# Kernel optimization log

Hardware: AMD Instinct MI355X
Metric: run time of the kernel (lower is better)

The kernel has to match this reference:

```python
import jax, jax.numpy as jnp
import numpy as np

N_NODES = 50000
N_EDGES = 800000
NUM_IN, NUM_HID, NUM_OUT = 512, 256, 64
EPS = 1e-12


def agnn_conv(x, src, dst, beta, num_nodes):
    # PyG AGNNConv: score(j->i) = beta * cos(x_i, x_j); softmax over incoming
    # edges of each target node i; out_i = sum_j alpha_ij * x_j.
    norm = jnp.maximum(jnp.linalg.norm(x, axis=1, keepdims=True), EPS)
    xn = x / norm                                      # [N, H]
    scores = beta * jnp.sum(xn[dst] * xn[src], axis=1)  # [E]
    m = jax.ops.segment_max(scores, dst, num_segments=num_nodes)
    e = jnp.exp(scores - m[dst])
    s = jax.ops.segment_sum(e, dst, num_segments=num_nodes)
    alpha = e / s[dst]                                  # [E]
    return jax.ops.segment_sum(alpha[:, None] * x[src], dst, num_segments=num_nodes)


def setup_inputs() -> dict:
    key = jax.random.key(0)
    ks = jax.random.split(key, 7)
    x = jax.random.normal(ks[0], (N_NODES, NUM_IN), dtype=jnp.float32)
    edge_index = jax.random.randint(ks[1], (2, N_EDGES), 0, N_NODES, dtype=jnp.int64)
    w1 = jax.random.normal(ks[2], (NUM_HID, NUM_IN), dtype=jnp.float32) / np.sqrt(NUM_IN)
    b1 = jnp.zeros((NUM_HID,), dtype=jnp.float32)
    beta2 = jnp.ones((1,), dtype=jnp.float32)
    w2 = jax.random.normal(ks[3], (NUM_OUT, NUM_HID), dtype=jnp.float32) / np.sqrt(NUM_HID)
    b2 = jnp.zeros((NUM_OUT,), dtype=jnp.float32)
    return {"x": x, "edge_index": edge_index, "w1": w1, "b1": b1,
            "beta2": beta2, "w2": w2, "b2": b2}


def reference(x, edge_index, w1, b1, beta2, w2, b2):
    n = x.shape[0]
    # add self-loops (PyG AGNNConv default add_self_loops=True)
    loops = jnp.arange(n, dtype=edge_index.dtype)
    src = jnp.concatenate([edge_index[0], loops])
    dst = jnp.concatenate([edge_index[1], loops])

    h = jax.nn.relu(x @ w1.T + b1)                       # [N, H] (eval: dropout = id)
    h = agnn_conv(h, src, dst, jnp.float32(1.0), n)      # prop1, fixed beta=1
    z1 = h
    h = agnn_conv(h, src, dst, beta2[0], n)              # prop2, learnable beta
    z2 = h
    logits = h @ w2.T + b2                               # [N, C]
    return (z1, z2, jax.nn.log_softmax(logits, axis=1))
```

## Files before the change

### kernel.cpp

```cpp
#include <hip/hip_runtime.h>

#define N_NODES 50000
#define N_EDGES 800000
#define ETOT (N_EDGES + N_NODES)
#define DIN 512
#define HID 256
#define NOUT 64
#define SCAN_CHUNK 2048

typedef __attribute__((ext_vector_type(8))) short short8;
typedef __attribute__((ext_vector_type(4))) float f32x4;
typedef __attribute__((ext_vector_type(4))) unsigned short us4;
typedef __attribute__((ext_vector_type(4))) unsigned int u32x4;

__device__ __forceinline__ unsigned short f2bf(float f) {
  union { float f; unsigned u; } x; x.f = f;
  unsigned r = x.u + 0x7fff + ((x.u >> 16) & 1);
  return (unsigned short)(r >> 16);
}
__device__ __forceinline__ float bf2f(unsigned short b) {
  return __uint_as_float(((unsigned)b) << 16);
}
__device__ __forceinline__ unsigned cvtpk(float a, float b) {
  unsigned r;
  asm("v_cvt_pk_bf16_f32 %0, %1, %2" : "=v"(r) : "v"(a), "v"(b));
  return r;
}

#define AS1(p) ((const __attribute__((address_space(1))) unsigned int*)(p))
#define AS3(p) ((__attribute__((address_space(3))) unsigned int*)(p))

__device__ __forceinline__ int edge_at(const void* ei, long long idx, int is32) {
  if (is32) return ((const int*)ei)[idx];
  return (int)((const long long*)ei)[idx];
}

__global__ void initK(const void* ei, int* cursor, int* flag,
                      const float* __restrict__ w1, unsigned short* __restrict__ wb) {
  int i = blockIdx.x * blockDim.x + threadIdx.x;
  if (i < N_NODES) cursor[i] = 1;
  if (i < (HID * DIN) / 8) {
    const float* src = w1 + i * 8;
    float4 v0 = ((const float4*)src)[0];
    float4 v1 = ((const float4*)src)[1];
    short8 s;
    s[0] = f2bf(v0.x); s[1] = f2bf(v0.y); s[2] = f2bf(v0.z); s[3] = f2bf(v0.w);
    s[4] = f2bf(v1.x); s[5] = f2bf(v1.y); s[6] = f2bf(v1.z); s[7] = f2bf(v1.w);
    *(short8*)(wb + i * 8) = s;
  }
  if (blockIdx.x == 0 && threadIdx.x < 64) {
    int lane = threadIdx.x;
    bool bad = false;
#pragma unroll
    for (int j = 0; j < 32; ++j) {
      long long v = ((const long long*)ei)[lane * 32 + j];
      bad |= (v < 0 || v >= N_NODES);
    }
    bool anybad = __any(bad);
    if (lane == 0) *flag = anybad ? 1 : 0;
  }
}

__global__ void histK(const void* ei, const int* flag, int* cursor) {
  int e = blockIdx.x * blockDim.x + threadIdx.x;
  if (e >= N_EDGES) return;
  int f = *flag;
  int d = edge_at(ei, (long long)N_EDGES + e, f);
  atomicAdd(&cursor[d], 1);
}

__global__ void scan1K(const int* counts, int* excl, int* bsums) {
  __shared__ int sdata[256];
  int base = blockIdx.x * SCAN_CHUNK;
  int t = threadIdx.x;
  int local[8];
  int sum = 0;
#pragma unroll
  for (int j = 0; j < 8; ++j) {
    int idx = base + t * 8 + j;
    int v = (idx < N_NODES) ? counts[idx] : 0;
    local[j] = sum;
    sum += v;
  }
  sdata[t] = sum;
  __syncthreads();
  for (int off = 1; off < 256; off <<= 1) {
    int v = (t >= off) ? sdata[t - off] : 0;
    __syncthreads();
    sdata[t] += v;
    __syncthreads();
  }
  int texcl = (t == 0) ? 0 : sdata[t - 1];
#pragma unroll
  for (int j = 0; j < 8; ++j) {
    int idx = base + t * 8 + j;
    if (idx < N_NODES) excl[idx] = texcl + local[j];
  }
  if (t == 255) bsums[blockIdx.x] = sdata[255];
}

__global__ void scan2K(int* bsums, int nb) {
  if (threadIdx.x == 0 && blockIdx.x == 0) {
    int run = 0;
    for (int i = 0; i < nb; ++i) { int v = bsums[i]; bsums[i] = run; run += v; }
  }
}

__global__ void scan3K(int* row_ptr, const int* bsums, int* cursor) {
  int i = blockIdx.x * blockDim.x + threadIdx.x;
  if (i < N_NODES) {
    int v = row_ptr[i] + bsums[i >> 11];
    row_ptr[i] = v;
    cursor[i] = v;
    if (i == 0) row_ptr[N_NODES] = ETOT;
  }
}

__global__ void scatterK(const void* ei, const int* flag, int* cursor, int* col) {
  int e = blockIdx.x * blockDim.x + threadIdx.x;
  if (e < N_EDGES) {
    int f = *flag;
    int s = edge_at(ei, e, f);
    int d = edge_at(ei, (long long)N_EDGES + e, f);
    int pos = atomicAdd(&cursor[d], 1);
    col[pos] = s;
  } else if (e < N_EDGES + N_NODES) {
    int i = e - N_EDGES;
    int pos = atomicAdd(&cursor[i], 1);
    col[pos] = i;
  }
}

__global__ __launch_bounds__(256) void gemm1MF(const float* __restrict__ A,
                                               const unsigned short* __restrict__ Bb,
                                               const float* __restrict__ bias,
                                               unsigned short* __restrict__ C) {
  __shared__ float As[128 * 64];
  __shared__ short Bs[128 * 64];
  int t = threadIdx.x;
  int wv = t >> 6, ln = t & 63;
  int wr = wv >> 1, wc = wv & 1;
  int row0 = blockIdx.x * 128;
  int col0 = blockIdx.y * 128;

  const float* aptr[8];
#pragma unroll
  for (int i = 0; i < 8; ++i) {
    int chunk = i * 4 + wv;
    int r = chunk * 4 + (ln >> 4);
    int gr = row0 + r;
    if (gr >= N_NODES) gr = N_NODES - 1;
    aptr[i] = &A[(long long)gr * DIN + (((ln & 15) ^ (r & 7)) << 2)];
  }
  const unsigned short* bptr[4];
#pragma unroll
  for (int i = 0; i < 4; ++i) {
    int chunk = i * 4 + wv;
    int r = chunk * 8 + (ln >> 3);
    bptr[i] = &Bb[(long long)(col0 + r) * DIN + (((ln & 7) ^ (r & 7)) << 3)];
  }

  f32x4 acc[4][4];
#pragma unroll
  for (int mi = 0; mi < 4; ++mi)
#pragma unroll
    for (int ni = 0; ni < 4; ++ni) acc[mi][ni] = (f32x4){0.f, 0.f, 0.f, 0.f};

  int g = ln >> 4;
  int fr = ln & 15;

  for (int k0 = 0; k0 < DIN; k0 += 64) {
#pragma unroll
    for (int i = 0; i < 8; ++i)
      __builtin_amdgcn_global_load_lds(AS1(aptr[i] + k0),
                                       AS3(&As[(i * 4 + wv) * 256]), 16, 0, 0);
#pragma unroll
    for (int i = 0; i < 4; ++i)
      __builtin_amdgcn_global_load_lds(AS1(bptr[i] + k0),
                                       AS3(&Bs[(i * 4 + wv) * 512]), 16, 0, 0);
    __syncthreads();

#pragma unroll
    for (int kk = 0; kk < 2; ++kk) {
      short8 af[4], bfr[4];
#pragma unroll
      for (int mi = 0; mi < 4; ++mi) {
        int r = wr * 64 + mi * 16 + fr;
        int s0 = kk * 8 + ((2 * g) ^ (r & 7));
        int s1 = kk * 8 + ((2 * g + 1) ^ (r & 7));
        f32x4 a0 = *(const f32x4*)&As[r * 64 + s0 * 4];
        f32x4 a1 = *(const f32x4*)&As[r * 64 + s1 * 4];
        u32x4 pk;
        pk.x = cvtpk(a0[0], a0[1]);
        pk.y = cvtpk(a0[2], a0[3]);
        pk.z = cvtpk(a1[0], a1[1]);
        pk.w = cvtpk(a1[2], a1[3]);
        af[mi] = __builtin_bit_cast(short8, pk);
      }
#pragma unroll
      for (int ni = 0; ni < 4; ++ni) {
        int c = wc * 64 + ni * 16 + fr;
        int slot = (kk * 4 + g) ^ (c & 7);
        bfr[ni] = *(const short8*)&Bs[c * 64 + slot * 8];
      }
#pragma unroll
      for (int mi = 0; mi < 4; ++mi)
#pragma unroll
        for (int ni = 0; ni < 4; ++ni)
          acc[mi][ni] = __builtin_amdgcn_mfma_f32_16x16x32_bf16(af[mi], bfr[ni], acc[mi][ni], 0, 0, 0);
    }
    __syncthreads();
  }

  int fq = ln >> 4;
#pragma unroll
  for (int ni = 0; ni < 4; ++ni) {
    int colv = col0 + wc * 64 + ni * 16 + fr;
    float bv = bias[colv];
#pragma unroll
    for (int mi = 0; mi < 4; ++mi) {
#pragma unroll
      for (int j = 0; j < 4; ++j) {
        int row = row0 + wr * 64 + mi * 16 + fq * 4 + j;
        if (row < N_NODES)
          C[(long long)row * HID + colv] = f2bf(fmaxf(acc[mi][ni][j] + bv, 0.f));
      }
    }
  }
}

__global__ __launch_bounds__(256) void normBF(const unsigned short* __restrict__ hb,
                                              float* __restrict__ invn) {
  int w = (blockIdx.x * 256 + threadIdx.x) >> 6;
  int lane = threadIdx.x & 63;
  if (w >= N_NODES) return;
  us4 v = *(const us4*)&hb[(long long)w * HID + lane * 4];
  float x = bf2f(v.x), y = bf2f(v.y), z = bf2f(v.z), ww = bf2f(v.w);
  float s = x * x + y * y + z * z + ww * ww;
#pragma unroll
  for (int off = 32; off >= 1; off >>= 1) s += __shfl_xor(s, off);
  if (lane == 0) invn[w] = 1.0f / fmaxf(sqrtf(s), 1e-12f);
}

__global__ __launch_bounds__(256) void convK(const unsigned short* __restrict__ hb,
                                             const float* __restrict__ invn,
                                             const int* __restrict__ row_ptr,
                                             const int* __restrict__ col,
                                             const float* __restrict__ beta_ptr,
                                             float* __restrict__ hout,
                                             unsigned short* __restrict__ hout_bf) {
  int w = (blockIdx.x * 256 + threadIdx.x) >> 6;
  int lane = threadIdx.x & 63;
  if (w >= N_NODES) return;
  int g = lane >> 4;
  int sub = lane & 15;
  float beta = beta_ptr ? beta_ptr[0] : 1.0f;
  float babs = fabsf(beta);

  const unsigned short* hrow = &hb[(long long)w * HID + sub * 16];
  short8 hia = *(const short8*)hrow;
  short8 hib = *(const short8*)(hrow + 8);
  float hi[16];
#pragma unroll
  for (int q = 0; q < 8; ++q) {
    hi[q] = bf2f((unsigned short)hia[q]);
    hi[8 + q] = bf2f((unsigned short)hib[q]);
  }
  float scale_i = invn[w] * beta;

  int e0 = row_ptr[w], e1 = row_ptr[w + 1];
  int nit = (e1 - e0 + 3) >> 2;
  float Z = 0.f;
  float acc[16];
#pragma unroll
  for (int q = 0; q < 16; ++q) acc[q] = 0.f;

  for (int it = 0; it < nit; ++it) {
    int ee = e0 + it * 4 + g;
    bool valid = ee < e1;
    int s = col[valid ? ee : (e1 - 1)];
    float is = invn[s];
    const unsigned short* hj = &hb[(long long)s * HID + sub * 16];
    short8 ja = *(const short8*)hj;
    short8 jb = *(const short8*)(hj + 8);
    float hjf[16];
#pragma unroll
    for (int q = 0; q < 8; ++q) {
      hjf[q] = bf2f((unsigned short)ja[q]);
      hjf[8 + q] = bf2f((unsigned short)jb[q]);
    }
    float p = 0.f;
#pragma unroll
    for (int q = 0; q < 16; ++q) p += hi[q] * hjf[q];
    p += __shfl_xor(p, 1);
    p += __shfl_xor(p, 2);
    p += __shfl_xor(p, 4);
    p += __shfl_xor(p, 8);
    float sc = p * scale_i * is;
    float wt = valid ? __expf(sc - babs) : 0.f;
    Z += wt;
#pragma unroll
    for (int q = 0; q < 16; ++q) acc[q] += wt * hjf[q];
  }

#pragma unroll
  for (int q = 0; q < 16; ++q) {
    acc[q] += __shfl_xor(acc[q], 16);
    acc[q] += __shfl_xor(acc[q], 32);
  }
  Z += __shfl_xor(Z, 16);
  Z += __shfl_xor(Z, 32);
  float r = 1.0f / Z;

  if (g == 0) {
    float* po = &hout[(long long)w * HID + sub * 16];
#pragma unroll
    for (int q4 = 0; q4 < 4; ++q4) {
      float4 o;
      o.x = acc[q4 * 4 + 0] * r;
      o.y = acc[q4 * 4 + 1] * r;
      o.z = acc[q4 * 4 + 2] * r;
      o.w = acc[q4 * 4 + 3] * r;
      *(float4*)&po[q4 * 4] = o;
    }
  } else if (g == 1 && hout_bf) {
    unsigned short* pb = &hout_bf[(long long)w * HID + sub * 16];
#pragma unroll
    for (int q4 = 0; q4 < 4; ++q4) {
      us4 ob;
      ob.x = f2bf(acc[q4 * 4 + 0] * r);
      ob.y = f2bf(acc[q4 * 4 + 1] * r);
      ob.z = f2bf(acc[q4 * 4 + 2] * r);
      ob.w = f2bf(acc[q4 * 4 + 3] * r);
      *(us4*)&pb[q4 * 4] = ob;
    }
  }
}

__global__ __launch_bounds__(256) void headK2(const float* __restrict__ Z,
                                              const float* __restrict__ W,
                                              const float* __restrict__ bias,
                                              float* __restrict__ out) {
  __shared__ float smem[2 * 32 * 68];
  float* As = smem;
  float* Bs = smem + 32 * 68;
  int t = threadIdx.x;
  int tx = t & 15, ty = t >> 4;
  int row0 = blockIdx.x * 64;
  float acc[4][4] = {};
  int lr = t >> 3;
  int lc4 = t & 7;

  for (int k0 = 0; k0 < HID; k0 += 32) {
#pragma unroll
    for (int rr = 0; rr < 64; rr += 32) {
      int gr = row0 + lr + rr;
      float4 va = (gr < N_NODES)
                      ? *(const float4*)&Z[(long long)gr * HID + k0 + lc4 * 4]
                      : make_float4(0.f, 0.f, 0.f, 0.f);
      As[(lc4 * 4 + 0) * 68 + lr + rr] = va.x;
      As[(lc4 * 4 + 1) * 68 + lr + rr] = va.y;
      As[(lc4 * 4 + 2) * 68 + lr + rr] = va.z;
      As[(lc4 * 4 + 3) * 68 + lr + rr] = va.w;
      int gc = lr + rr;
      float4 vb = *(const float4*)&W[(long long)gc * HID + k0 + lc4 * 4];
      Bs[(lc4 * 4 + 0) * 68 + lr + rr] = vb.x;
      Bs[(lc4 * 4 + 1) * 68 + lr + rr] = vb.y;
      Bs[(lc4 * 4 + 2) * 68 + lr + rr] = vb.z;
      Bs[(lc4 * 4 + 3) * 68 + lr + rr] = vb.w;
    }
    __syncthreads();
#pragma unroll
    for (int kk = 0; kk < 32; ++kk) {
      float4 a4 = *(const float4*)&As[kk * 68 + ty * 4];
      float4 b4 = *(const float4*)&Bs[kk * 68 + tx * 4];
      acc[0][0] += a4.x * b4.x; acc[0][1] += a4.x * b4.y; acc[0][2] += a4.x * b4.z; acc[0][3] += a4.x * b4.w;
      acc[1][0] += a4.y * b4.x; acc[1][1] += a4.y * b4.y; acc[1][2] += a4.y * b4.z; acc[1][3] += a4.y * b4.w;
      acc[2][0] += a4.z * b4.x; acc[2][1] += a4.z * b4.y; acc[2][2] += a4.z * b4.z; acc[2][3] += a4.z * b4.w;
      acc[3][0] += a4.w * b4.x; acc[3][1] += a4.w * b4.y; acc[3][2] += a4.w * b4.z; acc[3][3] += a4.w * b4.w;
    }
    __syncthreads();
  }

  float* ls = smem;
  float4 bv = *(const float4*)&bias[tx * 4];
#pragma unroll
  for (int r = 0; r < 4; ++r) {
    int lrow = ty * 4 + r;
    ls[lrow * 65 + tx * 4 + 0] = acc[r][0] + bv.x;
    ls[lrow * 65 + tx * 4 + 1] = acc[r][1] + bv.y;
    ls[lrow * 65 + tx * 4 + 2] = acc[r][2] + bv.z;
    ls[lrow * 65 + tx * 4 + 3] = acc[r][3] + bv.w;
  }
  __syncthreads();

  int wid = t >> 6, lane = t & 63;
#pragma unroll
  for (int rr2 = wid; rr2 < 64; rr2 += 4) {
    int node = row0 + rr2;
    if (node < N_NODES) {
      float v = ls[rr2 * 65 + lane];
      float mx = v;
#pragma unroll
      for (int off = 32; off >= 1; off >>= 1) mx = fmaxf(mx, __shfl_xor(mx, off));
      float ex = __expf(v - mx);
      float se = ex;
#pragma unroll
      for (int off = 32; off >= 1; off >>= 1) se += __shfl_xor(se, off);
      out[(long long)node * NOUT + lane] = v - mx - __logf(se);
    }
  }
}

extern "C" void kernel_launch(void* const* d_in, const int* in_sizes, int n_in,
                              void* d_out, int out_size, void* d_ws, size_t ws_size,
                              hipStream_t stream) {
  (void)in_sizes; (void)n_in; (void)out_size; (void)ws_size;
  const float* x = (const float*)d_in[0];
  const void* ei = d_in[1];
  const float* w1 = (const float*)d_in[2];
  const float* b1 = (const float*)d_in[3];
  const float* beta2 = (const float*)d_in[4];
  const float* w2 = (const float*)d_in[5];
  const float* b2 = (const float*)d_in[6];

  float* z1 = (float*)d_out;
  float* z2 = z1 + (size_t)N_NODES * HID;
  float* lsm = z2 + (size_t)N_NODES * HID;

  unsigned short* h_bf = (unsigned short*)d_ws;
  unsigned short* z1_bf = h_bf + (size_t)N_NODES * HID;
  float* invn = (float*)(z1_bf + (size_t)N_NODES * HID);
  int* row_ptr = (int*)(invn + N_NODES);
  int* cursor = row_ptr + N_NODES + 1;
  int* colv = cursor + N_NODES;
  int* bsums = colv + ETOT;
  int* flag = bsums + 64;
  unsigned short* wb = (unsigned short*)(flag + 4);

  int nScan = (N_NODES + SCAN_CHUNK - 1) / SCAN_CHUNK;

  initK<<<(N_NODES + 255) / 256, 256, 0, stream>>>(ei, cursor, flag, w1, wb);

  dim3 gg((N_NODES + 127) / 128, HID / 128);
  gemm1MF<<<gg, 256, 0, stream>>>(x, wb, b1, h_bf);

  histK<<<(N_EDGES + 255) / 256, 256, 0, stream>>>(ei, flag, cursor);
  scan1K<<<nScan, 256, 0, stream>>>(cursor, row_ptr, bsums);
  scan2K<<<1, 64, 0, stream>>>(bsums, nScan);
  scan3K<<<(N_NODES + 255) / 256, 256, 0, stream>>>(row_ptr, bsums, cursor);
  scatterK<<<(N_EDGES + N_NODES + 255) / 256, 256, 0, stream>>>(ei, flag, cursor, colv);

  normBF<<<(N_NODES + 3) / 4, 256, 0, stream>>>(h_bf, invn);
  convK<<<(N_NODES + 3) / 4, 256, 0, stream>>>(h_bf, invn, row_ptr, colv, nullptr, z1, z1_bf);
  normBF<<<(N_NODES + 3) / 4, 256, 0, stream>>>(z1_bf, invn);
  convK<<<(N_NODES + 3) / 4, 256, 0, stream>>>(z1_bf, invn, row_ptr, colv, beta2, z2, nullptr);

  headK2<<<(N_NODES + 63) / 64, 256, 0, stream>>>(z2, w2, b2, lsm);
}
```

Measured before the change: 361.7 us.

## Fuse row-norm into GEMM epilogue with full-width tiles; fold scan2 into scan3

The first GEMM now uses 64x256 tiles so each block owns complete hidden rows. That lets its epilogue compute the squared norm of the bf16-rounded output and write the inverse norm directly, so the separate normBF pass over h is dropped. The single-thread block-sum scan kernel is also removed, and each scan3 thread instead sums up to 24 preceding block totals itself. The cost is a different GEMM tile shape with more B traffic per block and an extra sync and LDS reduction, in exchange for two fewer launches and one fewer read of h.

```diff
diff --git a/kernel.cpp b/kernel.cpp
--- a/kernel.cpp
+++ b/kernel.cpp
@@ -99,17 +99,13 @@
   if (t == 255) bsums[blockIdx.x] = sdata[255];
 }
 
-__global__ void scan2K(int* bsums, int nb) {
-  if (threadIdx.x == 0 && blockIdx.x == 0) {
-    int run = 0;
-    for (int i = 0; i < nb; ++i) { int v = bsums[i]; bsums[i] = run; run += v; }
-  }
-}
-
 __global__ void scan3K(int* row_ptr, const int* bsums, int* cursor) {
   int i = blockIdx.x * blockDim.x + threadIdx.x;
   if (i < N_NODES) {
-    int v = row_ptr[i] + bsums[i >> 11];
+    int nb = i >> 11;
+    int pre = 0;
+    for (int b = 0; b < nb; ++b) pre += bsums[b];
+    int v = row_ptr[i] + pre;
     row_ptr[i] = v;
     cursor[i] = v;
     if (i == 0) row_ptr[N_NODES] = ETOT;
@@ -134,30 +130,30 @@
 __global__ __launch_bounds__(256) void gemm1MF(const float* __restrict__ A,
                                                const unsigned short* __restrict__ Bb,
                                                const float* __restrict__ bias,
-                                               unsigned short* __restrict__ C) {
-  __shared__ float As[128 * 64];
-  __shared__ short Bs[128 * 64];
+                                               unsigned short* __restrict__ C,
+                                               float* __restrict__ invn) {
+  __shared__ float As[64 * 64];
+  __shared__ short Bs[256 * 64];
   int t = threadIdx.x;
   int wv = t >> 6, ln = t & 63;
-  int wr = wv >> 1, wc = wv & 1;
-  int row0 = blockIdx.x * 128;
-  int col0 = blockIdx.y * 128;
-
-  const float* aptr[8];
-#pragma unroll
-  for (int i = 0; i < 8; ++i) {
+  int wc = wv;
+  int row0 = blockIdx.x * 64;
+
+  const float* aptr[4];
+#pragma unroll
+  for (int i = 0; i < 4; ++i) {
     int chunk = i * 4 + wv;
     int r = chunk * 4 + (ln >> 4);
     int gr = row0 + r;
     if (gr >= N_NODES) gr = N_NODES - 1;
     aptr[i] = &A[(long long)gr * DIN + (((ln & 15) ^ (r & 7)) << 2)];
   }
-  const unsigned short* bptr[4];
-#pragma unroll
-  for (int i = 0; i < 4; ++i) {
+  const unsigned short* bptr[8];
+#pragma unroll
+  for (int i = 0; i < 8; ++i) {
     int chunk = i * 4 + wv;
     int r = chunk * 8 + (ln >> 3);
-    bptr[i] = &Bb[(long long)(col0 + r) * DIN + (((ln & 7) ^ (r & 7)) << 3)];
+    bptr[i] = &Bb[(long long)r * DIN + (((ln & 7) ^ (r & 7)) << 3)];
   }
 
   f32x4 acc[4][4];
@@ -171,11 +167,11 @@
 
   for (int k0 = 0; k0 < DIN; k0 += 64) {
 #pragma unroll
-    for (int i = 0; i < 8; ++i)
+    for (int i = 0; i < 4; ++i)
       __builtin_amdgcn_global_load_lds(AS1(aptr[i] + k0),
                                        AS3(&As[(i * 4 + wv) * 256]), 16, 0, 0);
 #pragma unroll
-    for (int i = 0; i < 4; ++i)
+    for (int i = 0; i < 8; ++i)
       __builtin_amdgcn_global_load_lds(AS1(bptr[i] + k0),
                                        AS3(&Bs[(i * 4 + wv) * 512]), 16, 0, 0);
     __syncthreads();
@@ -185,7 +181,7 @@
       short8 af[4], bfr[4];
 #pragma unroll
       for (int mi = 0; mi < 4; ++mi) {
-        int r = wr * 64 + mi * 16 + fr;
+        int r = mi * 16 + fr;
         int s0 = kk * 8 + ((2 * g) ^ (r & 7));
         int s1 = kk * 8 + ((2 * g + 1) ^ (r & 7));
         f32x4 a0 = *(const f32x4*)&As[r * 64 + s0 * 4];
@@ -213,18 +209,54 @@
   }
 
   int fq = ln >> 4;
+  float ss[4][4];
+#pragma unroll
+  for (int mi = 0; mi < 4; ++mi)
+#pragma unroll
+    for (int j = 0; j < 4; ++j) ss[mi][j] = 0.f;
+
 #pragma unroll
   for (int ni = 0; ni < 4; ++ni) {
-    int colv = col0 + wc * 64 + ni * 16 + fr;
+    int colv = wc * 64 + ni * 16 + fr;
     float bv = bias[colv];
 #pragma unroll
     for (int mi = 0; mi < 4; ++mi) {
 #pragma unroll
       for (int j = 0; j < 4; ++j) {
-        int row = row0 + wr * 64 + mi * 16 + fq * 4 + j;
-        if (row < N_NODES)
-          C[(long long)row * HID + colv] = f2bf(fmaxf(acc[mi][ni][j] + bv, 0.f));
+        int row = row0 + mi * 16 + fq * 4 + j;
+        unsigned short us = f2bf(fmaxf(acc[mi][ni][j] + bv, 0.f));
+        if (row < N_NODES) C[(long long)row * HID + colv] = us;
+        float v = bf2f(us);
+        ss[mi][j] = fmaf(v, v, ss[mi][j]);
       }
+    }
+  }
+
+#pragma unroll
+  for (int mi = 0; mi < 4; ++mi)
+#pragma unroll
+    for (int j = 0; j < 4; ++j) {
+      float s = ss[mi][j];
+      s += __shfl_xor(s, 1);
+      s += __shfl_xor(s, 2);
+      s += __shfl_xor(s, 4);
+      s += __shfl_xor(s, 8);
+      ss[mi][j] = s;
+    }
+  float* redS = As;
+  if (fr == 0) {
+#pragma unroll
+    for (int mi = 0; mi < 4; ++mi)
+#pragma unroll
+      for (int j = 0; j < 4; ++j)
+        redS[(mi * 16 + fq * 4 + j) * 4 + wv] = ss[mi][j];
+  }
+  __syncthreads();
+  if (t < 64) {
+    int row = row0 + t;
+    if (row < N_NODES) {
+      float tot = redS[t * 4 + 0] + redS[t * 4 + 1] + redS[t * 4 + 2] + redS[t * 4 + 3];
+      invn[row] = 1.0f / fmaxf(sqrtf(tot), 1e-12f);
     }
   }
 }
@@ -442,16 +474,13 @@
 
   initK<<<(N_NODES + 255) / 256, 256, 0, stream>>>(ei, cursor, flag, w1, wb);
 
-  dim3 gg((N_NODES + 127) / 128, HID / 128);
-  gemm1MF<<<gg, 256, 0, stream>>>(x, wb, b1, h_bf);
+  gemm1MF<<<(N_NODES + 63) / 64, 256, 0, stream>>>(x, wb, b1, h_bf, invn);
 
   histK<<<(N_EDGES + 255) / 256, 256, 0, stream>>>(ei, flag, cursor);
   scan1K<<<nScan, 256, 0, stream>>>(cursor, row_ptr, bsums);
-  scan2K<<<1, 64, 0, stream>>>(bsums, nScan);
   scan3K<<<(N_NODES + 255) / 256, 256, 0, stream>>>(row_ptr, bsums, cursor);
   scatterK<<<(N_EDGES + N_NODES + 255) / 256, 256, 0, stream>>>(ei, flag, cursor, colv);
 
-  normBF<<<(N_NODES + 3) / 4, 256, 0, stream>>>(h_bf, invn);
   convK<<<(N_NODES + 3) / 4, 256, 0, stream>>>(h_bf, invn, row_ptr, colv, nullptr, z1, z1_bf);
   normBF<<<(N_NODES + 3) / 4, 256, 0, stream>>>(z1_bf, invn);
   convK<<<(N_NODES + 3) / 4, 256, 0, stream>>>(z1_bf, invn, row_ptr, colv, beta2, z2, nullptr);
```

New measurement: 340.0 us. 6.0% less time.
